# Performance work log

Measured on AMD Instinct MI355X. Metric: run time of the kernel, lower is better.

## Reference

```python
import jax, jax.numpy as jnp
from jax import lax
import numpy as np

B, T, D, H, OUT = 128, 1024, 256, 256, 2


def _rnn_layer(inp, W_xh, W_hh, b):
    # inp: [B, T, Din]; returns [B, T, H]
    h0 = jnp.zeros((inp.shape[0], W_hh.shape[0]), inp.dtype)

    def step(h, x_t):
        h_new = jnp.tanh(x_t @ W_xh.T + h @ W_hh.T + b)
        return h_new, h_new

    _, ys = lax.scan(step, h0, jnp.swapaxes(inp, 0, 1))  # ys: [T, B, H]
    return jnp.swapaxes(ys, 0, 1)


def setup_inputs() -> dict:
    key = jax.random.key(0)
    ks = jax.random.split(key, 8)
    s_in = 1.0 / np.sqrt(H)  # torch nn.RNN init scale
    x = jax.random.normal(ks[0], (B, T, D), dtype=jnp.float32)
    W_xh0 = jax.random.uniform(ks[1], (H, D), jnp.float32, -s_in, s_in)
    W_hh0 = jax.random.uniform(ks[2], (H, H), jnp.float32, -s_in, s_in)
    b0 = jax.random.uniform(ks[3], (H,), jnp.float32, -s_in, s_in)
    W_xh1 = jax.random.uniform(ks[4], (H, H), jnp.float32, -s_in, s_in)
    W_hh1 = jax.random.uniform(ks[5], (H, H), jnp.float32, -s_in, s_in)
    b1 = jax.random.uniform(ks[6], (H,), jnp.float32, -s_in, s_in)
    fc_w = jax.random.uniform(ks[7], (OUT, H), jnp.float32, -s_in, s_in)
    fc_b = jnp.zeros((OUT,), jnp.float32)
    return {"x": x, "W_xh0": W_xh0, "W_hh0": W_hh0, "b0": b0,
            "W_xh1": W_xh1, "W_hh1": W_hh1, "b1": b1,
            "fc_w": fc_w, "fc_b": fc_b}


def reference(x, W_xh0, W_hh0, b0, W_xh1, W_hh1, b1, fc_w, fc_b):
    h1 = _rnn_layer(x, W_xh0, W_hh0, b0)   # [B, T, H]
    h2 = _rnn_layer(h1, W_xh1, W_hh1, b1)  # [B, T, H]
    # linear head on last timestep
    return h2[:, -1, :] @ fc_w.T + fc_b    # [B, OUT]
```

## Files before the change

### kernel.cpp

```cpp
#include <hip/hip_runtime.h>

#define Bsz 128
#define Tn  1024
#define Dn  256
#define Hn  256

typedef _Float16 f16;
typedef _Float16 f16x4 __attribute__((ext_vector_type(4)));
typedef _Float16 f16x8 __attribute__((ext_vector_type(8)));
typedef float f32x4 __attribute__((ext_vector_type(4)));

__device__ __forceinline__ float tanh_fast(float x) {
    float e = __builtin_amdgcn_exp2f(x * 2.88539008177793f);
    return 1.0f - 2.0f * __builtin_amdgcn_rcpf(e + 1.0f);
}

__device__ __forceinline__ void wg_barrier() {
    asm volatile("s_waitcnt lgkmcnt(0)\n\ts_barrier" ::: "memory");
}


__global__ __launch_bounds__(256, 2) void k_xproj(
    const float* __restrict__ x, const float* __restrict__ W,
    const float* __restrict__ bias, float* __restrict__ preT)
{
    __shared__ __align__(16) f16 xt[128][264];
    const int tid = threadIdx.x;
    const int t = blockIdx.x;

    for (int i = tid; i < 128 * 64; i += 256) {
        int row = i >> 6, c4 = i & 63;
        float4 v = *(const float4*)(x + ((size_t)row * Tn + t) * Dn + c4 * 4);
        f16x4 tv = { (f16)v.x, (f16)v.y, (f16)v.z, (f16)v.w };
        *(f16x4*)(&xt[row][c4 * 4]) = tv;
    }

    const int lane = tid & 63, l15 = lane & 15, quad = lane >> 4;
    const int w = tid >> 6;

    f16x8 wf[4][8];
    #pragma unroll
    for (int jn = 0; jn < 4; jn++) {
        int j = w * 64 + jn * 16 + l15;
        #pragma unroll
        for (int kk = 0; kk < 8; kk++)
            #pragma unroll
            for (int e = 0; e < 8; e++)
                wf[jn][kk][e] = (f16)W[(size_t)j * Dn + kk * 32 + quad * 8 + e];
    }
    float4 bi[4];
    #pragma unroll
    for (int jn = 0; jn < 4; jn++)
        bi[jn] = *(const float4*)(bias + w * 64 + jn * 16 + quad * 4);

    __syncthreads();

    #pragma unroll 1
    for (int bblk = 0; bblk < 8; bblk++) {
        f32x4 acc[4];
        #pragma unroll
        for (int jn = 0; jn < 4; jn++)
            acc[jn] = (f32x4){bi[jn].x, bi[jn].y, bi[jn].z, bi[jn].w};
        #pragma unroll
        for (int kk = 0; kk < 8; kk++) {
            f16x8 xb = *(const f16x8*)(&xt[bblk * 16 + l15][kk * 32 + quad * 8]);
            #pragma unroll
            for (int jn = 0; jn < 4; jn++)
                acc[jn] = __builtin_amdgcn_mfma_f32_16x16x32_f16(wf[jn][kk], xb, acc[jn], 0, 0, 0);
        }
        #pragma unroll
        for (int jn = 0; jn < 4; jn++)
            #pragma unroll
            for (int r = 0; r < 4; r++) {
                int j = w * 64 + jn * 16 + quad * 4 + r;
                preT[((size_t)t * Hn + j) * Bsz + bblk * 16 + l15] = acc[jn][r];
            }
    }
}

__global__ __launch_bounds__(512, 2) void k_fused(
    const float* __restrict__ Whh0, const float* __restrict__ Wxh1,
    const float* __restrict__ Whh1, const float* __restrict__ b1v,
    const float* __restrict__ fcw,  const float* __restrict__ fcb,
    const float* __restrict__ preT, float* __restrict__ out)
{
    __shared__ __align__(16) f16 h1f[2][4096];
    __shared__ __align__(16) f16 h2f[2][4096];

    const int tid  = threadIdx.x;
    const int lane = tid & 63, l15 = lane & 15, quad = lane >> 4;
    const int w    = tid >> 6;
    const int colbase = w * 32;
    const int bg   = blockIdx.x * 16;

    for (int i = tid; i < 4096; i += 512) {
        h1f[0][i] = (f16)0.0f; h1f[1][i] = (f16)0.0f;
        h2f[0][i] = (f16)0.0f; h2f[1][i] = (f16)0.0f;
    }

    f16x8 wh0[2][8], wx[2][8], wh1[2][8];
    #pragma unroll
    for (int jn = 0; jn < 2; jn++) {
        int j = colbase + jn * 16 + l15;
        #pragma unroll
        for (int kk = 0; kk < 8; kk++)
            #pragma unroll
            for (int e = 0; e < 8; e++) {
                int o = (int)((size_t)j * Hn + kk * 32 + quad * 8 + e);
                wh0[jn][kk][e] = (f16)Whh0[o];
                wx [jn][kk][e] = (f16)Wxh1[o];
                wh1[jn][kk][e] = (f16)Whh1[o];
            }
    }
    float4 bi[2];
    #pragma unroll
    for (int jn = 0; jn < 2; jn++)
        bi[jn] = *(const float4*)(b1v + colbase + jn * 16 + quad * 4);

    int wroff[2];
    #pragma unroll
    for (int jn = 0; jn < 2; jn++) {
        int n0 = colbase + jn * 16 + quad * 4;
        wroff[jn] = (n0 >> 5) * 512 + ((n0 >> 3) & 3) * 128 + l15 * 8 + (n0 & 7);
    }

    float pn[8];
    #pragma unroll
    for (int jn = 0; jn < 2; jn++)
        #pragma unroll
        for (int r = 0; r < 4; r++) {
            int j = colbase + jn * 16 + quad * 4 + r;
            pn[jn * 4 + r] = preT[((size_t)0 * Hn + j) * Bsz + bg + l15];
        }
    __syncthreads();

#define FSTEP(P, TT) { \
     \
    f32x4 accA[2]; \
    _Pragma("unroll") for (int jn = 0; jn < 2; jn++) \
        _Pragma("unroll") for (int r = 0; r < 4; r++) accA[jn][r] = pn[jn*4+r]; \
    { int tf = ((TT) + 1 < Tn) ? (TT) + 1 : Tn - 1; \
      _Pragma("unroll") for (int jn = 0; jn < 2; jn++) \
          _Pragma("unroll") for (int r = 0; r < 4; r++) { \
              int j = colbase + jn * 16 + quad * 4 + r; \
              pn[jn*4+r] = preT[((size_t)tf * Hn + j) * Bsz + bg + l15]; } } \
    _Pragma("unroll") for (int kk = 0; kk < 8; kk++) { \
        f16x8 hb = *(const f16x8*)(&h1f[P][kk * 512 + lane * 8]); \
        accA[0] = __builtin_amdgcn_mfma_f32_16x16x32_f16(wh0[0][kk], hb, accA[0], 0, 0, 0); \
        accA[1] = __builtin_amdgcn_mfma_f32_16x16x32_f16(wh0[1][kk], hb, accA[1], 0, 0, 0); \
    } \
    _Pragma("unroll") for (int jn = 0; jn < 2; jn++) { \
        f16x4 t4 = { (f16)tanh_fast(accA[jn][0]), (f16)tanh_fast(accA[jn][1]), \
                     (f16)tanh_fast(accA[jn][2]), (f16)tanh_fast(accA[jn][3]) }; \
        *(f16x4*)(&h1f[1-(P)][wroff[jn]]) = t4; \
    } \
    wg_barrier();  \
     \
    f32x4 accB[2]; \
    _Pragma("unroll") for (int jn = 0; jn < 2; jn++) \
        accB[jn] = (f32x4){bi[jn].x, bi[jn].y, bi[jn].z, bi[jn].w}; \
    _Pragma("unroll") for (int kk = 0; kk < 8; kk++) { \
        f16x8 h1b = *(const f16x8*)(&h1f[1-(P)][kk * 512 + lane * 8]); \
        f16x8 h2b = *(const f16x8*)(&h2f[P][kk * 512 + lane * 8]); \
        accB[0] = __builtin_amdgcn_mfma_f32_16x16x32_f16(wx [0][kk], h1b, accB[0], 0, 0, 0); \
        accB[1] = __builtin_amdgcn_mfma_f32_16x16x32_f16(wx [1][kk], h1b, accB[1], 0, 0, 0); \
        accB[0] = __builtin_amdgcn_mfma_f32_16x16x32_f16(wh1[0][kk], h2b, accB[0], 0, 0, 0); \
        accB[1] = __builtin_amdgcn_mfma_f32_16x16x32_f16(wh1[1][kk], h2b, accB[1], 0, 0, 0); \
    } \
    _Pragma("unroll") for (int jn = 0; jn < 2; jn++) { \
        f16x4 t4 = { (f16)tanh_fast(accB[jn][0]), (f16)tanh_fast(accB[jn][1]), \
                     (f16)tanh_fast(accB[jn][2]), (f16)tanh_fast(accB[jn][3]) }; \
        *(f16x4*)(&h2f[1-(P)][wroff[jn]]) = t4; \
    } \
    wg_barrier();  \
}

    #pragma unroll 1
    for (int tp = 0; tp < Tn / 2; ++tp) {
        const int t0 = tp * 2;
        FSTEP(0, t0)
        FSTEP(1, (t0 + 1))
    }
#undef FSTEP

    if (tid < 256) {
        const int bl = tid >> 4, o = (tid >> 3) & 1, kc = tid & 7;
        float s = 0.f;
        #pragma unroll
        for (int kq = 0; kq < 32; kq++) {
            int k = kc * 32 + kq;
            f16 hv = h2f[0][(k >> 5) * 512 + ((k >> 3) & 3) * 128 + bl * 8 + (k & 7)];
            s += (float)hv * fcw[o * Hn + k];
        }
        s += __shfl_down(s, 4);
        s += __shfl_down(s, 2);
        s += __shfl_down(s, 1);
        if (kc == 0)
            out[(bg + bl) * 2 + o] = s + fcb[o];
    }
}

extern "C" void kernel_launch(void* const* d_in, const int* in_sizes, int n_in,
                              void* d_out, int out_size, void* d_ws, size_t ws_size,
                              hipStream_t stream) {
    const float* x    = (const float*)d_in[0];
    const float* Wxh0 = (const float*)d_in[1];
    const float* Whh0 = (const float*)d_in[2];
    const float* b0   = (const float*)d_in[3];
    const float* Wxh1 = (const float*)d_in[4];
    const float* Whh1 = (const float*)d_in[5];
    const float* b1   = (const float*)d_in[6];
    const float* fcw  = (const float*)d_in[7];
    const float* fcb  = (const float*)d_in[8];
    float* out = (float*)d_out;

    float* preT = (float*)d_ws;

    k_xproj<<<dim3(Tn),       dim3(256), 0, stream>>>(x, Wxh0, b0, preT);
    k_fused<<<dim3(Bsz / 16), dim3(512), 0, stream>>>(Whh0, Wxh1, Whh1, b1,
                                                      fcw, fcb, preT, out);
}
```

Baseline: 1.536 ms.

## Skew layer-2 recurrence one step behind layer 1 to halve barriers per step

Layer 2's step t-1 is computed in the same iteration as layer 1's step t, since both read the same h1 buffer. This wavefront skew removes one of the two workgroup barriers per timestep and lets the MFMA chains of both layers interleave, shortening the serial dependency path. Launch bounds drop to one block per CU to give room for the extra accumulators, and the final FC reads the other h2 buffer to match the new parity. The cost is an extra prologue step, an epilogue iteration, and higher register pressure.

```diff
diff --git a/kernel.cpp b/kernel.cpp
--- a/kernel.cpp
+++ b/kernel.cpp
@@ -78,7 +78,7 @@
     }
 }
 
-__global__ __launch_bounds__(512, 2) void k_fused(
+__global__ __launch_bounds__(512, 1) void k_fused(
     const float* __restrict__ Whh0, const float* __restrict__ Wxh1,
     const float* __restrict__ Whh1, const float* __restrict__ b1v,
     const float* __restrict__ fcw,  const float* __restrict__ fcb,
@@ -134,52 +134,53 @@
         }
     __syncthreads();
 
-#define FSTEP(P, TT) { \
-     \
-    f32x4 accA[2]; \
-    _Pragma("unroll") for (int jn = 0; jn < 2; jn++) \
+#define FSTEP(PR, I) { \
+    f32x4 accA[2], accX[2], accH[2]; \
+    _Pragma("unroll") for (int jn = 0; jn < 2; jn++) { \
         _Pragma("unroll") for (int r = 0; r < 4; r++) accA[jn][r] = pn[jn*4+r]; \
-    { int tf = ((TT) + 1 < Tn) ? (TT) + 1 : Tn - 1; \
+        accX[jn] = (f32x4){bi[jn].x, bi[jn].y, bi[jn].z, bi[jn].w}; \
+        accH[jn] = (f32x4){0.f, 0.f, 0.f, 0.f}; \
+    } \
+    { int tf = ((I) + 1 < Tn) ? (I) + 1 : Tn - 1; \
       _Pragma("unroll") for (int jn = 0; jn < 2; jn++) \
           _Pragma("unroll") for (int r = 0; r < 4; r++) { \
               int j = colbase + jn * 16 + quad * 4 + r; \
               pn[jn*4+r] = preT[((size_t)tf * Hn + j) * Bsz + bg + l15]; } } \
     _Pragma("unroll") for (int kk = 0; kk < 8; kk++) { \
-        f16x8 hb = *(const f16x8*)(&h1f[P][kk * 512 + lane * 8]); \
-        accA[0] = __builtin_amdgcn_mfma_f32_16x16x32_f16(wh0[0][kk], hb, accA[0], 0, 0, 0); \
-        accA[1] = __builtin_amdgcn_mfma_f32_16x16x32_f16(wh0[1][kk], hb, accA[1], 0, 0, 0); \
-    } \
-    _Pragma("unroll") for (int jn = 0; jn < 2; jn++) { \
-        f16x4 t4 = { (f16)tanh_fast(accA[jn][0]), (f16)tanh_fast(accA[jn][1]), \
-                     (f16)tanh_fast(accA[jn][2]), (f16)tanh_fast(accA[jn][3]) }; \
-        *(f16x4*)(&h1f[1-(P)][wroff[jn]]) = t4; \
-    } \
-    wg_barrier();  \
-     \
-    f32x4 accB[2]; \
-    _Pragma("unroll") for (int jn = 0; jn < 2; jn++) \
-        accB[jn] = (f32x4){bi[jn].x, bi[jn].y, bi[jn].z, bi[jn].w}; \
-    _Pragma("unroll") for (int kk = 0; kk < 8; kk++) { \
-        f16x8 h1b = *(const f16x8*)(&h1f[1-(P)][kk * 512 + lane * 8]); \
-        f16x8 h2b = *(const f16x8*)(&h2f[P][kk * 512 + lane * 8]); \
-        accB[0] = __builtin_amdgcn_mfma_f32_16x16x32_f16(wx [0][kk], h1b, accB[0], 0, 0, 0); \
-        accB[1] = __builtin_amdgcn_mfma_f32_16x16x32_f16(wx [1][kk], h1b, accB[1], 0, 0, 0); \
-        accB[0] = __builtin_amdgcn_mfma_f32_16x16x32_f16(wh1[0][kk], h2b, accB[0], 0, 0, 0); \
-        accB[1] = __builtin_amdgcn_mfma_f32_16x16x32_f16(wh1[1][kk], h2b, accB[1], 0, 0, 0); \
-    } \
-    _Pragma("unroll") for (int jn = 0; jn < 2; jn++) { \
-        f16x4 t4 = { (f16)tanh_fast(accB[jn][0]), (f16)tanh_fast(accB[jn][1]), \
-                     (f16)tanh_fast(accB[jn][2]), (f16)tanh_fast(accB[jn][3]) }; \
-        *(f16x4*)(&h2f[1-(P)][wroff[jn]]) = t4; \
-    } \
-    wg_barrier();  \
-}
-
+        f16x8 hb1 = *(const f16x8*)(&h1f[(PR)^1][kk * 512 + lane * 8]); \
+        f16x8 hb2 = *(const f16x8*)(&h2f[(PR)  ][kk * 512 + lane * 8]); \
+        accA[0] = __builtin_amdgcn_mfma_f32_16x16x32_f16(wh0[0][kk], hb1, accA[0], 0, 0, 0); \
+        accA[1] = __builtin_amdgcn_mfma_f32_16x16x32_f16(wh0[1][kk], hb1, accA[1], 0, 0, 0); \
+        accX[0] = __builtin_amdgcn_mfma_f32_16x16x32_f16(wx [0][kk], hb1, accX[0], 0, 0, 0); \
+        accX[1] = __builtin_amdgcn_mfma_f32_16x16x32_f16(wx [1][kk], hb1, accX[1], 0, 0, 0); \
+        accH[0] = __builtin_amdgcn_mfma_f32_16x16x32_f16(wh1[0][kk], hb2, accH[0], 0, 0, 0); \
+        accH[1] = __builtin_amdgcn_mfma_f32_16x16x32_f16(wh1[1][kk], hb2, accH[1], 0, 0, 0); \
+    } \
+    if ((I) < Tn) { \
+        _Pragma("unroll") for (int jn = 0; jn < 2; jn++) { \
+            f16x4 t4 = { (f16)tanh_fast(accA[jn][0]), (f16)tanh_fast(accA[jn][1]), \
+                         (f16)tanh_fast(accA[jn][2]), (f16)tanh_fast(accA[jn][3]) }; \
+            *(f16x4*)(&h1f[(PR)][wroff[jn]]) = t4; \
+        } \
+    } \
+    if ((I) > 0) { \
+        _Pragma("unroll") for (int jn = 0; jn < 2; jn++) { \
+            f16x4 t4 = { (f16)tanh_fast(accX[jn][0] + accH[jn][0]), \
+                         (f16)tanh_fast(accX[jn][1] + accH[jn][1]), \
+                         (f16)tanh_fast(accX[jn][2] + accH[jn][2]), \
+                         (f16)tanh_fast(accX[jn][3] + accH[jn][3]) }; \
+            *(f16x4*)(&h2f[(PR)^1][wroff[jn]]) = t4; \
+        } \
+    } \
+    wg_barrier(); \
+}
+
+    FSTEP(0, 0)
     #pragma unroll 1
     for (int tp = 0; tp < Tn / 2; ++tp) {
-        const int t0 = tp * 2;
-        FSTEP(0, t0)
-        FSTEP(1, (t0 + 1))
+        const int i1 = 2 * tp + 1;
+        FSTEP(1, i1)
+        FSTEP(0, (i1 + 1))
     }
 #undef FSTEP
 
@@ -189,7 +190,7 @@
         #pragma unroll
         for (int kq = 0; kq < 32; kq++) {
             int k = kc * 32 + kq;
-            f16 hv = h2f[0][(k >> 5) * 512 + ((k >> 3) & 3) * 128 + bl * 8 + (k & 7)];
+            f16 hv = h2f[1][(k >> 5) * 512 + ((k >> 3) & 3) * 128 + bl * 8 + (k & 7)];
             s += (float)hv * fcw[o * Hn + k];
         }
         s += __shfl_down(s, 4);
```

Measured after the change: 1.701 ms. 10.7% more time.
